# Optimization experiments

Hardware: AMD Instinct MI355X
Metric: run time of the kernel (lower is better)

## Reference

```python
import jax, jax.numpy as jnp
import numpy as np

BS, L, D, H, DC = 8, 8192, 128, 128, 128
C_CONST = 8.0  # rg-lru temperature constant


def _ln(x):
    # LayerNorm without scale/bias (use_bias=False, use_scale=False)
    m = jnp.mean(x, axis=-1, keepdims=True)
    v = jnp.mean(jnp.square(x - m), axis=-1, keepdims=True)
    return (x - m) * jax.lax.rsqrt(v + 1e-6)


def _affine(c, w, b):
    # Dense(features=1)(c)[:, :, None] -> (bs, 1, 1) broadcast scalar per sequence
    return (c @ w + b)[:, :, None]


def _combine(e1, e2):
    a1, b1 = e1
    a2, b2 = e2
    return (a1 * a2, a2 * b1 + b2)


def _linear_scan(a, b, reverse):
    # h_t = a_t * h_{t-1} + b_t (or h_{t+1} when reverse) along seq axis 1
    _, h = jax.lax.associative_scan(_combine, (a, b), axis=1, reverse=reverse)
    return h


def _forward(x, c, cln1_sw, cln1_sb, cln1_bw, cln1_bb, gate1_w, gate1_b,
             rnn_in_w, rnn_in_b, pos_emb, rnn_wi, rnn_bi, rnn_wr, rnn_br, rnn_a,
             rnn_out_w, rnn_out_b, cln2_sw, cln2_sb, cln2_bw, cln2_bb,
             gate2_w, gate2_b, mlp_w1, mlp_b1, mlp_w2, mlp_b2):
    # --- branch 1: conditioned LN -> bidirectional RG-LRU -> gated residual ---
    h = (1.0 + _affine(c, cln1_sw, cln1_sb)) * _ln(x) + _affine(c, cln1_bw, cln1_bb)
    u = _ln(h) @ rnn_in_w + rnn_in_b + pos_emb[None]          # (bs, L, H)
    gi = jax.nn.sigmoid(u @ rnn_wi + rnn_bi)                   # input gate
    gr = jax.nn.sigmoid(u @ rnn_wr + rnn_br)                   # recurrence gate
    at = jnp.exp(C_CONST * gr * jnp.log(rnn_a))                # a_t = a^(c*r_t)
    bt = jnp.sqrt(1.0 - jnp.square(at)) * (gi * u)
    hf = _linear_scan(at, bt, reverse=False)
    hb = _linear_scan(at, bt, reverse=True)
    r = jnp.concatenate([hf, hb], axis=-1) @ rnn_out_w + rnn_out_b  # (bs, L, D)
    x = x + _affine(c, gate1_w, gate1_b) * r
    # --- branch 2: conditioned LN -> gelu MLP -> gated residual ---
    h = (1.0 + _affine(c, cln2_sw, cln2_sb)) * _ln(x) + _affine(c, cln2_bw, cln2_bb)
    m = jax.nn.gelu(h @ mlp_w1 + mlp_b1) @ mlp_w2 + mlp_b2
    return x + _affine(c, gate2_w, gate2_b) * m


def setup_inputs() -> dict:
    key = jax.random.key(0)
    ks = jax.random.split(key, 30)
    def n(k, shape, s=0.05):
        return (jax.random.normal(k, shape) * s).astype(jnp.float32)
    rnn_a = (0.9 + 0.09 * jax.random.uniform(ks[0], (H,))).astype(jnp.float32)
    return {
        "x": jax.random.normal(ks[1], (BS, L, D), jnp.float32),
        "c": jax.random.normal(ks[2], (BS, DC), jnp.float32),
        "cln1_sw": n(ks[3], (DC, 1)), "cln1_sb": n(ks[4], (1,)),
        "cln1_bw": n(ks[5], (DC, 1)), "cln1_bb": n(ks[6], (1,)),
        "gate1_w": n(ks[7], (DC, 1)), "gate1_b": n(ks[8], (1,)),
        "rnn_in_w": n(ks[9], (D, H), 0.1), "rnn_in_b": n(ks[10], (H,)),
        "pos_emb": n(ks[11], (L, H), 0.02),
        "rnn_wi": n(ks[12], (H, H), 0.1), "rnn_bi": n(ks[13], (H,)),
        "rnn_wr": n(ks[14], (H, H), 0.1), "rnn_br": n(ks[15], (H,)),
        "rnn_a": rnn_a,
        "rnn_out_w": n(ks[16], (2 * H, D), 0.1), "rnn_out_b": n(ks[17], (D,)),
        "cln2_sw": n(ks[18], (DC, 1)), "cln2_sb": n(ks[19], (1,)),
        "cln2_bw": n(ks[20], (DC, 1)), "cln2_bb": n(ks[21], (1,)),
        "gate2_w": n(ks[22], (DC, 1)), "gate2_b": n(ks[23], (1,)),
        "mlp_w1": n(ks[24], (D, 4 * D), 0.1), "mlp_b1": n(ks[25], (4 * D,)),
        "mlp_w2": n(ks[26], (4 * D, D), 0.1), "mlp_b2": n(ks[27], (D,)),
    }


def reference(x, c, cln1_sw, cln1_sb, cln1_bw, cln1_bb, gate1_w, gate1_b,
              rnn_in_w, rnn_in_b, pos_emb, rnn_wi, rnn_bi, rnn_wr, rnn_br, rnn_a,
              rnn_out_w, rnn_out_b, cln2_sw, cln2_sb, cln2_bw, cln2_bb,
              gate2_w, gate2_b, mlp_w1, mlp_b1, mlp_w2, mlp_b2):
    return _forward(x, c, cln1_sw, cln1_sb, cln1_bw, cln1_bb, gate1_w, gate1_b,
                    rnn_in_w, rnn_in_b, pos_emb, rnn_wi, rnn_bi, rnn_wr, rnn_br, rnn_a,
                    rnn_out_w, rnn_out_b, cln2_sw, cln2_sb, cln2_bw, cln2_bb,
                    gate2_w, gate2_b, mlp_w1, mlp_b1, mlp_w2, mlp_b2)
```

## Files before the change

### kernel.cpp

```cpp
#include <hip/hip_runtime.h>
#include <hip/hip_bf16.h>

#define BSZ 8
#define SEQ 8192
#define DIM 128
#define NCH 128
#define CLEN 64

typedef unsigned short u16;
typedef unsigned int u32;
typedef short bf16x8 __attribute__((ext_vector_type(8)));
typedef float f32x4  __attribute__((ext_vector_type(4)));
typedef float f32x16 __attribute__((ext_vector_type(16)));

__device__ __forceinline__ float us2f(u16 w){ union{u32 i;float f;}u; u.i=((u32)w)<<16; return u.f; }
__device__ __forceinline__ u16 f2us(float f){
  __hip_bfloat16 h = __float2bfloat16(f);
  union{ __hip_bfloat16 b; u16 s; }u; u.b=h; return u.s;
}
__device__ __forceinline__ float wred64(float v){
  #pragma unroll
  for (int o=1;o<64;o<<=1) v += __shfl_xor(v,o,64);
  return v;
}
__device__ __forceinline__ float red16(float v){
  v += __shfl_xor(v,1,64); v += __shfl_xor(v,2,64);
  v += __shfl_xor(v,4,64); v += __shfl_xor(v,8,64);
  return v;
}
__device__ __forceinline__ float sigmoidf_(float z){ return 1.f/(1.f+__expf(-z)); }
__device__ __forceinline__ float gelu_tanh(float x){
  float y = 0.7978845608028654f * fmaf(0.044715f*x, x*x, x);
  float e = __expf(2.f*y);
  float th = 1.f - 2.f/(e+1.f);
  return 0.5f*x*(1.f+th);
}
__device__ __forceinline__ void lds_fence(){
  asm volatile("s_waitcnt lgkmcnt(0)" ::: "memory");
  __builtin_amdgcn_sched_barrier(0);
}

__global__ __launch_bounds__(64) void k_aff(
    const float* __restrict__ c,
    const float* w0,const float* w1,const float* w2,const float* w3,const float* w4,const float* w5,
    const float* s0,const float* s1,const float* s2,const float* s3,const float* s4,const float* s5,
    float* __restrict__ aff)
{
  const float* ws[6]={w0,w1,w2,w3,w4,w5};
  const float* bs[6]={s0,s1,s2,s3,s4,s5};
  int l = threadIdx.x;
  for (int b=0;b<BSZ;++b){
    #pragma unroll
    for (int h=0;h<6;++h){
      float v = c[b*128+l]*ws[h][l] + c[b*128+64+l]*ws[h][64+l];
      v = wred64(v);
      if (l==0) aff[b*6+h] = v + bs[h][0];
    }
  }
}

__device__ __forceinline__ void pack_one(const float* __restrict__ W, int N,
                                         u16* __restrict__ out, int fi)
{
  int lane = fi & 63;
  int k2   = (fi >> 6) & 1;
  int cn   = fi >> 7;
  int NB   = N >> 4;
  int n    = cn % NB, c = cn / NB;
  int k0   = c*64 + k2*32 + (lane>>4)*8;
  int col  = n*16 + (lane&15);
  u16* o = out + (size_t)fi*8;
  #pragma unroll
  for (int j=0;j<8;++j) o[j] = f2us(W[(size_t)(k0+j)*N + col]);
}

__device__ __forceinline__ void pack32A(const float* __restrict__ W, int N,
                                        u16* __restrict__ out, int fi)
{
  int lane = fi & 63;
  int ks   = (fi >> 6) & 7;
  int ng   = fi >> 9;
  int k0   = ks*16 + (lane>>5)*8;
  int col  = ng*32 + (lane&31);
  u16* o = out + (size_t)fi*8;
  #pragma unroll
  for (int j=0;j<8;++j) o[j] = f2us(W[(size_t)(k0+j)*N + col]);
}

__device__ __forceinline__ void pack32B(const float* __restrict__ W, int N,
                                        u16* __restrict__ out, int fi)
{
  int lane = fi & 63;
  int ot   = (fi >> 6) & 3;
  int ksg  = fi >> 8;
  int k0   = ksg*16 + (lane>>5)*8;
  int col  = ot*32 + (lane&31);
  u16* o = out + (size_t)fi*8;
  #pragma unroll
  for (int j=0;j<8;++j) o[j] = f2us(W[(size_t)(k0+j)*N + col]);
}

__global__ __launch_bounds__(256) void k_prep(
    const float* __restrict__ w1, const float* __restrict__ w2, const float* __restrict__ wo,
    const float* __restrict__ win, const float* __restrict__ wi, const float* __restrict__ wr,
    u16* __restrict__ w1t, u16* __restrict__ w2t, u16* __restrict__ wot,
    u16* __restrict__ wint, u16* __restrict__ wit, u16* __restrict__ wrt)
{
  int i = blockIdx.x*256 + threadIdx.x;
  if      (i <  8192) pack32A(w1, 512, w1t, i);
  else if (i < 16384) pack32B(w2, 128, w2t, i-8192);
  else if (i < 20480) pack_one(wo, 128, wot, i-16384);
  else if (i < 22528) pack_one(win,128, wint,i-20480);
  else if (i < 24576) pack_one(wi, 128, wit, i-22528);
  else                pack_one(wr, 128, wrt, i-24576);
}

__global__ __launch_bounds__(256,4) void k_pre(
    const float* __restrict__ xg, const u16* __restrict__ wint, const float* __restrict__ b_in,
    const float* __restrict__ pos, const u16* __restrict__ wit, const float* __restrict__ b_i,
    const u16* __restrict__ wrt, const float* __restrict__ b_r, const float* __restrict__ avec,
    const float* __restrict__ aff,
    u32* __restrict__ abg,
    float* __restrict__ Ag, float* __restrict__ Bfg, float* __restrict__ Bbg)
{
  __shared__ __align__(16) u32 abp[CLEN*DIM];
  u16* A_l = (u16*)abp;
  const int t  = threadIdx.x;
  const int b  = blockIdx.x >> 7;
  const int ck = blockIdx.x & (NCH-1);
  const size_t base = ((size_t)(b*SEQ + ck*CLEN))*DIM;
  const int lane=t&63, wv=t>>6, col=lane&15, quad=lane>>4;
  const int m0 = wv*16;

  {
    const float s1p = 1.f + aff[b*6+0];
    const int cg=t&15, rg=t>>4, j0=cg*8, r0=rg*4;
    #pragma unroll
    for (int ii=0;ii<4;++ii){
      int r=r0+ii;
      const float* xo = xg + base + (size_t)r*DIM + j0;
      float4 a = *(const float4*)xo;
      float4 bq = *(const float4*)(xo+4);
      float o[8]={a.x,a.y,a.z,a.w,bq.x,bq.y,bq.z,bq.w};
      float s=0.f;
      #pragma unroll
      for (int j=0;j<8;++j) s+=o[j];
      s=red16(s); float m=s*(1.f/128.f);
      float q2=0.f;
      #pragma unroll
      for (int j=0;j<8;++j){ float d=o[j]-m; q2+=d*d; }
      q2=red16(q2); float var=q2*(1.f/128.f);
      float rs=rsqrtf(var+1e-6f);
      float vz=var*rs*rs;
      float tt2=s1p*rsqrtf(fmaf(s1p*s1p,vz,1e-6f));
      float sc=rs*tt2;
      u32 pk[4];
      #pragma unroll
      for (int q=0;q<4;++q){
        pk[q]= (u32)f2us((o[2*q]-m)*sc) | ((u32)f2us((o[2*q+1]-m)*sc)<<16);
      }
      *(uint4*)&A_l[r*136+j0] = make_uint4(pk[0],pk[1],pk[2],pk[3]);
    }
  }
  lds_fence();

  f32x4 uacc[8];
  #pragma unroll
  for (int n=0;n<8;++n) uacc[n]=(f32x4){0.f,0.f,0.f,0.f};
  #pragma unroll
  for (int c=0;c<2;++c){
    #pragma unroll
    for (int k2=0;k2<2;++k2){
      bf16x8 av = *(const bf16x8*)&A_l[(m0+col)*136 + c*64 + k2*32 + quad*8];
      #pragma unroll
      for (int n=0;n<8;++n){
        bf16x8 bv = *(const bf16x8*)&wint[(size_t)(((c*8+n)*2+k2)*64+lane)*8];
        uacc[n] = __builtin_amdgcn_mfma_f32_16x16x32_bf16(av, bv, uacc[n], 0,0,0);
      }
    }
  }
  float u_c[8][4];
  #pragma unroll
  for (int n=0;n<8;++n){
    int nc = n*16 + col;
    float bi = b_in[nc];
    #pragma unroll
    for (int r=0;r<4;++r){
      int row = m0 + quad*4 + r;
      u_c[n][r] = uacc[n][r] + bi + pos[(size_t)(ck*CLEN+row)*DIM + nc];
    }
  }
  #pragma unroll
  for (int n=0;n<8;++n){
    #pragma unroll
    for (int r=0;r<4;++r)
      A_l[(m0+quad*4+r)*136 + n*16+col] = f2us(u_c[n][r]);
  }
  lds_fence();

  f32x4 gacc[8], racc[8];
  #pragma unroll
  for (int n=0;n<8;++n){ gacc[n]=(f32x4){0.f,0.f,0.f,0.f}; racc[n]=(f32x4){0.f,0.f,0.f,0.f}; }
  #pragma unroll
  for (int c=0;c<2;++c){
    #pragma unroll
    for (int k2=0;k2<2;++k2){
      bf16x8 av = *(const bf16x8*)&A_l[(m0+col)*136 + c*64 + k2*32 + quad*8];
      #pragma unroll
      for (int n=0;n<8;++n){
        bf16x8 bgi = *(const bf16x8*)&wit[(size_t)(((c*8+n)*2+k2)*64+lane)*8];
        gacc[n] = __builtin_amdgcn_mfma_f32_16x16x32_bf16(av, bgi, gacc[n], 0,0,0);
        bf16x8 bgr = *(const bf16x8*)&wrt[(size_t)(((c*8+n)*2+k2)*64+lane)*8];
        racc[n] = __builtin_amdgcn_mfma_f32_16x16x32_bf16(av, bgr, racc[n], 0,0,0);
      }
    }
  }
  __syncthreads();

  #pragma unroll
  for (int n=0;n<8;++n){
    int nc = n*16 + col;
    float la = __logf(avec[nc]);
    float br = b_r[nc];
    float bi = b_i[nc];
    #pragma unroll
    for (int r=0;r<4;++r){
      int row = m0 + quad*4 + r;
      float gi = sigmoidf_(gacc[n][r]+bi);
      float g  = sigmoidf_(racc[n][r]+br);
      float a  = __expf(8.f*g*la);
      float bb = sqrtf(fmaxf(1.f-a*a,0.f))*gi*u_c[n][r];
      abp[row*DIM+nc] = (u32)f2us(a) | ((u32)f2us(bb)<<16);
    }
  }
  __syncthreads();

  {
    uint4* dst = (uint4*)(abg + base);
    const uint4* src = (const uint4*)abp;
    #pragma unroll
    for (int i=t;i<2048;i+=256) dst[i]=src[i];
  }

  const int sbase = (b*NCH+ck)*DIM;
  if (t < 128){
    float h=0.f, p=1.f;
    #pragma unroll 4
    for (int tt=0;tt<CLEN;++tt){
      u32 v=abp[tt*DIM+t];
      float a=us2f((u16)v), bb=us2f((u16)(v>>16));
      h=fmaf(a,h,bb); p*=a;
    }
    Ag[sbase+t]=p; Bfg[sbase+t]=h;
  } else {
    int ch=t-128; float h=0.f;
    #pragma unroll 4
    for (int tt=CLEN-1;tt>=0;--tt){
      u32 v=abp[tt*DIM+ch];
      h=fmaf(us2f((u16)v),h,us2f((u16)(v>>16)));
    }
    Bbg[sbase+ch]=h;
  }
}

__global__ __launch_bounds__(1024) void k_chunkscan(
    const float* __restrict__ Ag, const float* __restrict__ Bfg, const float* __restrict__ Bbg,
    float* __restrict__ Hf, float* __restrict__ Hb)
{
  __shared__ float sP[8][128], sS[8][128];
  const int dir = blockIdx.x >> 3, b = blockIdx.x & 7;
  const int t = threadIdx.x, seg = t>>7, ch = t&127;
  const size_t cbase = (size_t)b*NCH*DIM + ch;
  float P=1.f, S=0.f;
  if (dir==0){
    #pragma unroll 4
    for (int j=0;j<16;++j){
      size_t i = cbase + (size_t)(seg*16+j)*DIM;
      float a=Ag[i]; S=fmaf(a,S,Bfg[i]); P*=a;
    }
  } else {
    #pragma unroll 4
    for (int j=15;j>=0;--j){
      size_t i = cbase + (size_t)(seg*16+j)*DIM;
      float a=Ag[i]; S=fmaf(a,S,Bbg[i]); P*=a;
    }
  }
  sP[seg][ch]=P; sS[seg][ch]=S;
  __syncthreads();
  float h=0.f;
  if (dir==0){ for (int s=0;s<seg;++s) h=fmaf(sP[s][ch],h,sS[s][ch]); }
  else       { for (int s=7;s>seg;--s) h=fmaf(sP[s][ch],h,sS[s][ch]); }
  if (dir==0){
    #pragma unroll 4
    for (int j=0;j<16;++j){
      size_t i = cbase + (size_t)(seg*16+j)*DIM;
      Hf[i]=h; h=fmaf(Ag[i],h,Bfg[i]);
    }
  } else {
    #pragma unroll 4
    for (int j=15;j>=0;--j){
      size_t i = cbase + (size_t)(seg*16+j)*DIM;
      Hb[i]=h; h=fmaf(Ag[i],h,Bbg[i]);
    }
  }
}

__global__ __launch_bounds__(256,4) void k_scan(
    const u32* __restrict__ abg,
    const float* __restrict__ Hf, const float* __restrict__ Hb,
    const float* __restrict__ xg, const u16* __restrict__ wot, const float* __restrict__ b_out,
    const float* __restrict__ aff, float* __restrict__ outg)
{
  __shared__ __align__(16) u16 hcat[CLEN*264];
  const int t  = threadIdx.x;
  const int b  = blockIdx.x >> 7;
  const int ck = blockIdx.x & (NCH-1);
  const size_t base = ((size_t)(b*SEQ + ck*CLEN))*DIM;
  const int pbase=(b*NCH+ck)*DIM;

  if (t<128){
    const u32* p = abg + base + t;
    float h = Hf[pbase+t];
    u32 v0=p[0], v1=p[128], v2=p[256], v3=p[384];
    #pragma unroll
    for (int g=0; g<16; ++g){
      u32 n0=0,n1=0,n2=0,n3=0;
      if (g<15){
        n0=p[(g*4+4)*128]; n1=p[(g*4+5)*128];
        n2=p[(g*4+6)*128]; n3=p[(g*4+7)*128];
      }
      h=fmaf(us2f((u16)v0),h,us2f((u16)(v0>>16))); hcat[(g*4+0)*264+t]=f2us(h);
      h=fmaf(us2f((u16)v1),h,us2f((u16)(v1>>16))); hcat[(g*4+1)*264+t]=f2us(h);
      h=fmaf(us2f((u16)v2),h,us2f((u16)(v2>>16))); hcat[(g*4+2)*264+t]=f2us(h);
      h=fmaf(us2f((u16)v3),h,us2f((u16)(v3>>16))); hcat[(g*4+3)*264+t]=f2us(h);
      v0=n0; v1=n1; v2=n2; v3=n3;
    }
  } else {
    int ch=t-128;
    const u32* p = abg + base + ch;
    float h = Hb[pbase+ch];
    u32 v0=p[63*128], v1=p[62*128], v2=p[61*128], v3=p[60*128];
    #pragma unroll
    for (int g=0; g<16; ++g){
      u32 n0=0,n1=0,n2=0,n3=0;
      if (g<15){
        n0=p[(59-g*4)*128]; n1=p[(58-g*4)*128];
        n2=p[(57-g*4)*128]; n3=p[(56-g*4)*128];
      }
      h=fmaf(us2f((u16)v0),h,us2f((u16)(v0>>16))); hcat[(63-g*4)*264+128+ch]=f2us(h);
      h=fmaf(us2f((u16)v1),h,us2f((u16)(v1>>16))); hcat[(62-g*4)*264+128+ch]=f2us(h);
      h=fmaf(us2f((u16)v2),h,us2f((u16)(v2>>16))); hcat[(61-g*4)*264+128+ch]=f2us(h);
      h=fmaf(us2f((u16)v3),h,us2f((u16)(v3>>16))); hcat[(60-g*4)*264+128+ch]=f2us(h);
      v0=n0; v1=n1; v2=n2; v3=n3;
    }
  }
  __syncthreads();

  const int lane=t&63, wv=t>>6, col=lane&15, quad=lane>>4;
  const int m0 = wv*16;
  f32x4 acc[8];
  #pragma unroll
  for (int n=0;n<8;++n) acc[n]=(f32x4){0.f,0.f,0.f,0.f};
  #pragma unroll
  for (int chk=0; chk<4; ++chk){
    #pragma unroll
    for (int k2=0;k2<2;++k2){
      bf16x8 av = *(const bf16x8*)&hcat[(m0+col)*264 + chk*64 + k2*32 + quad*8];
      #pragma unroll
      for (int n=0;n<8;++n){
        bf16x8 bv = *(const bf16x8*)&wot[(size_t)(((chk*8+n)*2+k2)*64+lane)*8];
        acc[n] = __builtin_amdgcn_mfma_f32_16x16x32_bf16(av, bv, acc[n], 0,0,0);
      }
    }
  }
  __syncthreads();
  float* pbuf = (float*)hcat;
  #pragma unroll
  for (int n=0;n<8;++n){
    #pragma unroll
    for (int r=0;r<4;++r)
      pbuf[(m0+quad*4+r)*128 + n*16+col] = acc[n][r];
  }
  __syncthreads();

  const float g1=aff[b*6+2];
  const float4* xv4 = (const float4*)(xg+base);
  float4* ov4 = (float4*)(outg+base);
  const float4* cv4 = (const float4*)pbuf;
  #pragma unroll
  for (int i=t;i<2048;i+=256){
    float4 cv = cv4[i];
    float4 xv = xv4[i];
    float4 bo = *(const float4*)&b_out[(i*4)&127];
    float4 r;
    r.x=fmaf(g1,cv.x+bo.x,xv.x); r.y=fmaf(g1,cv.y+bo.y,xv.y);
    r.z=fmaf(g1,cv.z+bo.z,xv.z); r.w=fmaf(g1,cv.w+bo.w,xv.w);
    ov4[i]=r;
  }
}

__global__ __launch_bounds__(256,2) void k_mlp(
    const u16* __restrict__ w1t, const float* __restrict__ b1v,
    const u16* __restrict__ w2t, const float* __restrict__ b2v,
    const float* __restrict__ aff, float* __restrict__ outg)
{
  __shared__ __align__(16) u32 smem4[8192];
  u16* h2l = (u16*)smem4;
  const int t=threadIdx.x;
  const int b=blockIdx.x>>7;
  const size_t base=(size_t)blockIdx.x*CLEN*DIM;
  const int lane=t&63, wv=t>>6;
  const int l31=lane&31, h5=lane>>5;
  const float s2p=1.f+aff[b*6+3], b2a=aff[b*6+4], g2=aff[b*6+5];

  {
    const int cg=t&15, rg=t>>4, j0=cg*8, r0=rg*4;
    #pragma unroll
    for (int ii=0;ii<4;++ii){
      int r=r0+ii;
      const float* xo = outg + base + (size_t)r*DIM + j0;
      float4 a = *(const float4*)xo;
      float4 bq = *(const float4*)(xo+4);
      float o[8]={a.x,a.y,a.z,a.w,bq.x,bq.y,bq.z,bq.w};
      float s=0.f;
      #pragma unroll
      for (int j=0;j<8;++j) s+=o[j];
      s=red16(s); float m=s*(1.f/128.f);
      float q2=0.f;
      #pragma unroll
      for (int j=0;j<8;++j){ float d=o[j]-m; q2+=d*d; }
      q2=red16(q2); float rs=rsqrtf(q2*(1.f/128.f)+1e-6f);
      u32 pk[4];
      #pragma unroll
      for (int q=0;q<4;++q){
        float a0=fmaf((o[2*q]-m)*rs,   s2p, b2a);
        float a1=fmaf((o[2*q+1]-m)*rs, s2p, b2a);
        pk[q]= (u32)f2us(a0) | ((u32)f2us(a1)<<16);
      }
      *(uint4*)&h2l[r*136+j0] = make_uint4(pk[0],pk[1],pk[2],pk[3]);
    }
  }
  __syncthreads();

  f32x16 acc2[2][4];
  #pragma unroll
  for (int m=0;m<2;++m)
    #pragma unroll
    for (int n=0;n<4;++n)
      #pragma unroll
      for (int r=0;r<16;++r) acc2[m][n][r]=0.f;

  for (int nt=0;nt<4;++nt){
    bf16x8 w1A[8];
    #pragma unroll
    for (int ks=0;ks<8;++ks)
      w1A[ks] = *(const bf16x8*)&w1t[((size_t)((wv*4+nt)*8 + ks)*64 + lane)*8];
    #pragma unroll
    for (int tt=0;tt<2;++tt){
      f32x16 a1;
      #pragma unroll
      for (int r=0;r<16;++r) a1[r]=0.f;
      #pragma unroll
      for (int ks=0;ks<8;++ks){
        bf16x8 hb = *(const bf16x8*)&h2l[(tt*32 + l31)*136 + ks*16 + h5*8];
        a1 = __builtin_amdgcn_mfma_f32_32x32x16_bf16(w1A[ks], hb, a1, 0,0,0);
      }
      u32 pk[8];
      #pragma unroll
      for (int q=0;q<4;++q){
        float4 bq = *(const float4*)&b1v[wv*128 + nt*32 + q*8 + h5*4];
        float g0=gelu_tanh(a1[4*q+0]+bq.x);
        float g1=gelu_tanh(a1[4*q+1]+bq.y);
        float g2_=gelu_tanh(a1[4*q+2]+bq.z);
        float g3=gelu_tanh(a1[4*q+3]+bq.w);
        pk[2*q+0]=(u32)f2us(g0)|((u32)f2us(g1)<<16);
        pk[2*q+1]=(u32)f2us(g2_)|((u32)f2us(g3)<<16);
      }
      asm volatile("v_permlane32_swap_b32 %0, %1" : "+v"(pk[0]), "+v"(pk[2]));
      asm volatile("v_permlane32_swap_b32 %0, %1" : "+v"(pk[1]), "+v"(pk[3]));
      asm volatile("v_permlane32_swap_b32 %0, %1" : "+v"(pk[4]), "+v"(pk[6]));
      asm volatile("v_permlane32_swap_b32 %0, %1" : "+v"(pk[5]), "+v"(pk[7]));
      union F8 { bf16x8 v; u32 u[4]; } A0, A1;
      A0.u[0]=pk[0]; A0.u[1]=pk[1]; A0.u[2]=pk[2]; A0.u[3]=pk[3];
      A1.u[0]=pk[4]; A1.u[1]=pk[5]; A1.u[2]=pk[6]; A1.u[3]=pk[7];
      #pragma unroll
      for (int ot=0;ot<4;++ot){
        bf16x8 wb0 = *(const bf16x8*)&w2t[((size_t)((wv*8 + nt*2 + 0)*4 + ot)*64 + lane)*8];
        acc2[tt][ot] = __builtin_amdgcn_mfma_f32_32x32x16_bf16(A0.v, wb0, acc2[tt][ot], 0,0,0);
        bf16x8 wb1 = *(const bf16x8*)&w2t[((size_t)((wv*8 + nt*2 + 1)*4 + ot)*64 + lane)*8];
        acc2[tt][ot] = __builtin_amdgcn_mfma_f32_32x32x16_bf16(A1.v, wb1, acc2[tt][ot], 0,0,0);
      }
    }
  }
  __syncthreads();

  float* pbuf = (float*)smem4;
  const int lrow = (lane>>4)&3;
  const int cb   = (lane&15)*8;
  #pragma unroll
  for (int rt=0;rt<4;++rt){
    const int tt = rt>>1, gg = rt&1;
    if (rt) __syncthreads();
    #pragma unroll
    for (int ot=0;ot<4;++ot){
      #pragma unroll
      for (int q=0;q<2;++q){
        #pragma unroll
        for (int r=0;r<4;++r){
          int reg = gg*8 + q*4 + r;
          int tl  = q*8 + r + 4*h5;
          pbuf[wv*2048 + tl*128 + ot*32 + l31] = acc2[tt][ot][reg];
        }
      }
    }
    __syncthreads();
    float s[8] = {0.f,0.f,0.f,0.f,0.f,0.f,0.f,0.f};
    #pragma unroll
    for (int p=0;p<4;++p){
      float4 x0 = *(const float4*)&pbuf[p*2048 + (4*wv+lrow)*128 + cb];
      float4 x1 = *(const float4*)&pbuf[p*2048 + (4*wv+lrow)*128 + cb + 4];
      s[0]+=x0.x; s[1]+=x0.y; s[2]+=x0.z; s[3]+=x0.w;
      s[4]+=x1.x; s[5]+=x1.y; s[6]+=x1.z; s[7]+=x1.w;
    }
    int grow = rt*16 + 4*wv + lrow;
    size_t gi = base + (size_t)grow*DIM + cb;
    float4 o0 = *(const float4*)&outg[gi];
    float4 o1 = *(const float4*)&outg[gi+4];
    float4 bb0 = *(const float4*)&b2v[cb];
    float4 bb1 = *(const float4*)&b2v[cb+4];
    float4 r0, r1;
    r0.x = fmaf(g2, s[0]+bb0.x, o0.x); r0.y = fmaf(g2, s[1]+bb0.y, o0.y);
    r0.z = fmaf(g2, s[2]+bb0.z, o0.z); r0.w = fmaf(g2, s[3]+bb0.w, o0.w);
    r1.x = fmaf(g2, s[4]+bb1.x, o1.x); r1.y = fmaf(g2, s[5]+bb1.y, o1.y);
    r1.z = fmaf(g2, s[6]+bb1.z, o1.z); r1.w = fmaf(g2, s[7]+bb1.w, o1.w);
    *(float4*)&outg[gi]   = r0;
    *(float4*)&outg[gi+4] = r1;
  }
}

extern "C" void kernel_launch(void* const* d_in, const int* in_sizes, int n_in,
                              void* d_out, int out_size, void* d_ws, size_t ws_size,
                              hipStream_t stream)
{
  (void)in_sizes; (void)n_in; (void)out_size; (void)ws_size;
  const float* x   =(const float*)d_in[0];
  const float* c   =(const float*)d_in[1];
  const float* c1sw=(const float*)d_in[2];  const float* c1sb=(const float*)d_in[3];
  const float* c1bw=(const float*)d_in[4];  const float* c1bb=(const float*)d_in[5];
  const float* g1w =(const float*)d_in[6];  const float* g1b =(const float*)d_in[7];
  const float* win =(const float*)d_in[8];  const float* binv=(const float*)d_in[9];
  const float* pos =(const float*)d_in[10];
  const float* wi  =(const float*)d_in[11]; const float* biv =(const float*)d_in[12];
  const float* wr  =(const float*)d_in[13]; const float* brv =(const float*)d_in[14];
  const float* av  =(const float*)d_in[15];
  const float* wout=(const float*)d_in[16]; const float* bout=(const float*)d_in[17];
  const float* c2sw=(const float*)d_in[18]; const float* c2sb=(const float*)d_in[19];
  const float* c2bw=(const float*)d_in[20]; const float* c2bb=(const float*)d_in[21];
  const float* g2w =(const float*)d_in[22]; const float* g2b =(const float*)d_in[23];
  const float* w1  =(const float*)d_in[24]; const float* b1v =(const float*)d_in[25];
  const float* w2  =(const float*)d_in[26]; const float* b2v =(const float*)d_in[27];

  float* wsf  = (float*)d_ws;
  float* Ag   = wsf;
  float* Bfg  = Ag   + 131072;
  float* Bbg  = Bfg  + 131072;
  float* Hf   = Bbg  + 131072;
  float* Hb   = Hf   + 131072;
  float* aff  = Hb   + 131072;
  u16*   w1t  = (u16*)(aff + 64);
  u16*   w2t  = w1t + 65536;
  u16*   wot  = w2t + 65536;
  u16*   wint = wot + 32768;
  u16*   wit  = wint + 16384;
  u16*   wrt  = wit  + 16384;
  u32*   abg  = (u32*)(wrt + 16384);

  float* outg = (float*)d_out;

  k_aff<<<dim3(1),dim3(64),0,stream>>>(c, c1sw,c1bw,g1w,c2sw,c2bw,g2w,
                                       c1sb,c1bb,g1b,c2sb,c2bb,g2b, aff);
  k_prep<<<dim3(104),dim3(256),0,stream>>>(w1,w2,wout,win,wi,wr,
                                           w1t,w2t,wot,wint,wit,wrt);
  k_pre<<<dim3(BSZ*NCH),dim3(256),0,stream>>>(x,wint,binv,pos,wit,biv,wrt,brv,av,aff,
                                              abg, Ag,Bfg,Bbg);
  k_chunkscan<<<dim3(16),dim3(1024),0,stream>>>(Ag,Bfg,Bbg,Hf,Hb);
  k_scan<<<dim3(BSZ*NCH),dim3(256),0,stream>>>(abg,Hf,Hb,x,wot,bout,aff,outg);
  k_mlp<<<dim3(BSZ*NCH),dim3(256),0,stream>>>(w1t,b1v,w2t,b2v,aff,outg);
}
```

Measured before the change: 272.6 us.

## Restructure MLP kernel so each wave owns 32 rows with full hidden dim

The MLP kernel now gives each wave 32 rows and loops over all 512 hidden units, instead of splitting the hidden dimension across waves. This removes the cross-wave LDS reduction and its block barriers, and the residual is written straight from the accumulators. Each block covers 128 rows, so half as many blocks are launched. The affine kernel is also folded into the weight-prep launch as an extra block, saving one launch. The cost is that each wave now reads the whole W1/W2 from global/L2, which is more weight traffic per row, and the output stores are scattered at float granularity.

```diff
diff --git a/kernel.cpp b/kernel.cpp
--- a/kernel.cpp
+++ b/kernel.cpp
@@ -38,25 +38,6 @@
 __device__ __forceinline__ void lds_fence(){
   asm volatile("s_waitcnt lgkmcnt(0)" ::: "memory");
   __builtin_amdgcn_sched_barrier(0);
-}
-
-__global__ __launch_bounds__(64) void k_aff(
-    const float* __restrict__ c,
-    const float* w0,const float* w1,const float* w2,const float* w3,const float* w4,const float* w5,
-    const float* s0,const float* s1,const float* s2,const float* s3,const float* s4,const float* s5,
-    float* __restrict__ aff)
-{
-  const float* ws[6]={w0,w1,w2,w3,w4,w5};
-  const float* bs[6]={s0,s1,s2,s3,s4,s5};
-  int l = threadIdx.x;
-  for (int b=0;b<BSZ;++b){
-    #pragma unroll
-    for (int h=0;h<6;++h){
-      float v = c[b*128+l]*ws[h][l] + c[b*128+64+l]*ws[h][64+l];
-      v = wred64(v);
-      if (l==0) aff[b*6+h] = v + bs[h][0];
-    }
-  }
 }
 
 __device__ __forceinline__ void pack_one(const float* __restrict__ W, int N,
@@ -104,8 +85,28 @@
     const float* __restrict__ w1, const float* __restrict__ w2, const float* __restrict__ wo,
     const float* __restrict__ win, const float* __restrict__ wi, const float* __restrict__ wr,
     u16* __restrict__ w1t, u16* __restrict__ w2t, u16* __restrict__ wot,
-    u16* __restrict__ wint, u16* __restrict__ wit, u16* __restrict__ wrt)
-{
+    u16* __restrict__ wint, u16* __restrict__ wit, u16* __restrict__ wrt,
+    const float* __restrict__ c,
+    const float* a0,const float* a1,const float* a2,const float* a3,const float* a4,const float* a5,
+    const float* s0,const float* s1,const float* s2,const float* s3,const float* s4,const float* s5,
+    float* __restrict__ aff)
+{
+  if (blockIdx.x == 104){
+    int l = threadIdx.x;
+    if (l < 64){
+      const float* ws[6]={a0,a1,a2,a3,a4,a5};
+      const float* bs[6]={s0,s1,s2,s3,s4,s5};
+      for (int b=0;b<BSZ;++b){
+        #pragma unroll
+        for (int h=0;h<6;++h){
+          float v = c[b*128+l]*ws[h][l] + c[b*128+64+l]*ws[h][64+l];
+          v = wred64(v);
+          if (l==0) aff[b*6+h] = v + bs[h][0];
+        }
+      }
+    }
+    return;
+  }
   int i = blockIdx.x*256 + threadIdx.x;
   if      (i <  8192) pack32A(w1, 512, w1t, i);
   else if (i < 16384) pack32B(w2, 128, w2t, i-8192);
@@ -404,21 +405,22 @@
     const u16* __restrict__ w2t, const float* __restrict__ b2v,
     const float* __restrict__ aff, float* __restrict__ outg)
 {
-  __shared__ __align__(16) u32 smem4[8192];
-  u16* h2l = (u16*)smem4;
+  __shared__ __align__(16) u16 h2l[4*32*136];
   const int t=threadIdx.x;
-  const int b=blockIdx.x>>7;
-  const size_t base=(size_t)blockIdx.x*CLEN*DIM;
+  const int b=blockIdx.x>>6;
+  const size_t base=(size_t)blockIdx.x*128*DIM;
   const int lane=t&63, wv=t>>6;
   const int l31=lane&31, h5=lane>>5;
   const float s2p=1.f+aff[b*6+3], b2a=aff[b*6+4], g2=aff[b*6+5];
+  u16* h2w = h2l + wv*32*136;
+  const size_t wbase = base + (size_t)wv*32*DIM;
 
   {
-    const int cg=t&15, rg=t>>4, j0=cg*8, r0=rg*4;
-    #pragma unroll
-    for (int ii=0;ii<4;++ii){
-      int r=r0+ii;
-      const float* xo = outg + base + (size_t)r*DIM + j0;
+    const int cg=lane&15, rg=lane>>4, j0=cg*8;
+    #pragma unroll
+    for (int ii=0;ii<8;++ii){
+      int r=rg*8+ii;
+      const float* xo = outg + wbase + (size_t)r*DIM + j0;
       float4 a = *(const float4*)xo;
       float4 bq = *(const float4*)(xo+4);
       float o[8]={a.x,a.y,a.z,a.w,bq.x,bq.y,bq.z,bq.w};
@@ -437,104 +439,68 @@
         float a1=fmaf((o[2*q+1]-m)*rs, s2p, b2a);
         pk[q]= (u32)f2us(a0) | ((u32)f2us(a1)<<16);
       }
-      *(uint4*)&h2l[r*136+j0] = make_uint4(pk[0],pk[1],pk[2],pk[3]);
-    }
-  }
-  __syncthreads();
-
-  f32x16 acc2[2][4];
-  #pragma unroll
-  for (int m=0;m<2;++m)
-    #pragma unroll
-    for (int n=0;n<4;++n)
-      #pragma unroll
-      for (int r=0;r<16;++r) acc2[m][n][r]=0.f;
-
-  for (int nt=0;nt<4;++nt){
+      *(uint4*)&h2w[r*136+j0] = make_uint4(pk[0],pk[1],pk[2],pk[3]);
+    }
+  }
+  lds_fence();
+
+  f32x16 acc2[4];
+  #pragma unroll
+  for (int n=0;n<4;++n)
+    #pragma unroll
+    for (int r=0;r<16;++r) acc2[n][r]=0.f;
+
+  for (int nt=0;nt<16;++nt){
     bf16x8 w1A[8];
     #pragma unroll
     for (int ks=0;ks<8;++ks)
-      w1A[ks] = *(const bf16x8*)&w1t[((size_t)((wv*4+nt)*8 + ks)*64 + lane)*8];
-    #pragma unroll
-    for (int tt=0;tt<2;++tt){
-      f32x16 a1;
-      #pragma unroll
-      for (int r=0;r<16;++r) a1[r]=0.f;
-      #pragma unroll
-      for (int ks=0;ks<8;++ks){
-        bf16x8 hb = *(const bf16x8*)&h2l[(tt*32 + l31)*136 + ks*16 + h5*8];
-        a1 = __builtin_amdgcn_mfma_f32_32x32x16_bf16(w1A[ks], hb, a1, 0,0,0);
-      }
-      u32 pk[8];
-      #pragma unroll
-      for (int q=0;q<4;++q){
-        float4 bq = *(const float4*)&b1v[wv*128 + nt*32 + q*8 + h5*4];
-        float g0=gelu_tanh(a1[4*q+0]+bq.x);
-        float g1=gelu_tanh(a1[4*q+1]+bq.y);
-        float g2_=gelu_tanh(a1[4*q+2]+bq.z);
-        float g3=gelu_tanh(a1[4*q+3]+bq.w);
-        pk[2*q+0]=(u32)f2us(g0)|((u32)f2us(g1)<<16);
-        pk[2*q+1]=(u32)f2us(g2_)|((u32)f2us(g3)<<16);
-      }
-      asm volatile("v_permlane32_swap_b32 %0, %1" : "+v"(pk[0]), "+v"(pk[2]));
-      asm volatile("v_permlane32_swap_b32 %0, %1" : "+v"(pk[1]), "+v"(pk[3]));
-      asm volatile("v_permlane32_swap_b32 %0, %1" : "+v"(pk[4]), "+v"(pk[6]));
-      asm volatile("v_permlane32_swap_b32 %0, %1" : "+v"(pk[5]), "+v"(pk[7]));
-      union F8 { bf16x8 v; u32 u[4]; } A0, A1;
-      A0.u[0]=pk[0]; A0.u[1]=pk[1]; A0.u[2]=pk[2]; A0.u[3]=pk[3];
-      A1.u[0]=pk[4]; A1.u[1]=pk[5]; A1.u[2]=pk[6]; A1.u[3]=pk[7];
-      #pragma unroll
-      for (int ot=0;ot<4;++ot){
-        bf16x8 wb0 = *(const bf16x8*)&w2t[((size_t)((wv*8 + nt*2 + 0)*4 + ot)*64 + lane)*8];
-        acc2[tt][ot] = __builtin_amdgcn_mfma_f32_32x32x16_bf16(A0.v, wb0, acc2[tt][ot], 0,0,0);
-        bf16x8 wb1 = *(const bf16x8*)&w2t[((size_t)((wv*8 + nt*2 + 1)*4 + ot)*64 + lane)*8];
-        acc2[tt][ot] = __builtin_amdgcn_mfma_f32_32x32x16_bf16(A1.v, wb1, acc2[tt][ot], 0,0,0);
-      }
-    }
-  }
-  __syncthreads();
-
-  float* pbuf = (float*)smem4;
-  const int lrow = (lane>>4)&3;
-  const int cb   = (lane&15)*8;
-  #pragma unroll
-  for (int rt=0;rt<4;++rt){
-    const int tt = rt>>1, gg = rt&1;
-    if (rt) __syncthreads();
+      w1A[ks] = *(const bf16x8*)&w1t[((size_t)(nt*8 + ks)*64 + lane)*8];
+    f32x16 a1a, a1b;
+    #pragma unroll
+    for (int r=0;r<16;++r){ a1a[r]=0.f; a1b[r]=0.f; }
+    #pragma unroll
+    for (int ks=0;ks<4;++ks){
+      bf16x8 hb0 = *(const bf16x8*)&h2w[l31*136 + (2*ks+0)*16 + h5*8];
+      a1a = __builtin_amdgcn_mfma_f32_32x32x16_bf16(w1A[2*ks+0], hb0, a1a, 0,0,0);
+      bf16x8 hb1 = *(const bf16x8*)&h2w[l31*136 + (2*ks+1)*16 + h5*8];
+      a1b = __builtin_amdgcn_mfma_f32_32x32x16_bf16(w1A[2*ks+1], hb1, a1b, 0,0,0);
+    }
+    u32 pk[8];
+    #pragma unroll
+    for (int q=0;q<4;++q){
+      float4 bq = *(const float4*)&b1v[nt*32 + q*8 + h5*4];
+      float g0=gelu_tanh(a1a[4*q+0]+a1b[4*q+0]+bq.x);
+      float g1=gelu_tanh(a1a[4*q+1]+a1b[4*q+1]+bq.y);
+      float g2_=gelu_tanh(a1a[4*q+2]+a1b[4*q+2]+bq.z);
+      float g3=gelu_tanh(a1a[4*q+3]+a1b[4*q+3]+bq.w);
+      pk[2*q+0]=(u32)f2us(g0)|((u32)f2us(g1)<<16);
+      pk[2*q+1]=(u32)f2us(g2_)|((u32)f2us(g3)<<16);
+    }
+    asm volatile("v_permlane32_swap_b32 %0, %1" : "+v"(pk[0]), "+v"(pk[2]));
+    asm volatile("v_permlane32_swap_b32 %0, %1" : "+v"(pk[1]), "+v"(pk[3]));
+    asm volatile("v_permlane32_swap_b32 %0, %1" : "+v"(pk[4]), "+v"(pk[6]));
+    asm volatile("v_permlane32_swap_b32 %0, %1" : "+v"(pk[5]), "+v"(pk[7]));
+    union F8 { bf16x8 v; u32 u[4]; } A0, A1;
+    A0.u[0]=pk[0]; A0.u[1]=pk[1]; A0.u[2]=pk[2]; A0.u[3]=pk[3];
+    A1.u[0]=pk[4]; A1.u[1]=pk[5]; A1.u[2]=pk[6]; A1.u[3]=pk[7];
     #pragma unroll
     for (int ot=0;ot<4;++ot){
-      #pragma unroll
-      for (int q=0;q<2;++q){
-        #pragma unroll
-        for (int r=0;r<4;++r){
-          int reg = gg*8 + q*4 + r;
-          int tl  = q*8 + r + 4*h5;
-          pbuf[wv*2048 + tl*128 + ot*32 + l31] = acc2[tt][ot][reg];
-        }
-      }
-    }
-    __syncthreads();
-    float s[8] = {0.f,0.f,0.f,0.f,0.f,0.f,0.f,0.f};
-    #pragma unroll
-    for (int p=0;p<4;++p){
-      float4 x0 = *(const float4*)&pbuf[p*2048 + (4*wv+lrow)*128 + cb];
-      float4 x1 = *(const float4*)&pbuf[p*2048 + (4*wv+lrow)*128 + cb + 4];
-      s[0]+=x0.x; s[1]+=x0.y; s[2]+=x0.z; s[3]+=x0.w;
-      s[4]+=x1.x; s[5]+=x1.y; s[6]+=x1.z; s[7]+=x1.w;
-    }
-    int grow = rt*16 + 4*wv + lrow;
-    size_t gi = base + (size_t)grow*DIM + cb;
-    float4 o0 = *(const float4*)&outg[gi];
-    float4 o1 = *(const float4*)&outg[gi+4];
-    float4 bb0 = *(const float4*)&b2v[cb];
-    float4 bb1 = *(const float4*)&b2v[cb+4];
-    float4 r0, r1;
-    r0.x = fmaf(g2, s[0]+bb0.x, o0.x); r0.y = fmaf(g2, s[1]+bb0.y, o0.y);
-    r0.z = fmaf(g2, s[2]+bb0.z, o0.z); r0.w = fmaf(g2, s[3]+bb0.w, o0.w);
-    r1.x = fmaf(g2, s[4]+bb1.x, o1.x); r1.y = fmaf(g2, s[5]+bb1.y, o1.y);
-    r1.z = fmaf(g2, s[6]+bb1.z, o1.z); r1.w = fmaf(g2, s[7]+bb1.w, o1.w);
-    *(float4*)&outg[gi]   = r0;
-    *(float4*)&outg[gi+4] = r1;
+      bf16x8 wb0 = *(const bf16x8*)&w2t[((size_t)((nt*2 + 0)*4 + ot)*64 + lane)*8];
+      acc2[ot] = __builtin_amdgcn_mfma_f32_32x32x16_bf16(A0.v, wb0, acc2[ot], 0,0,0);
+      bf16x8 wb1 = *(const bf16x8*)&w2t[((size_t)((nt*2 + 1)*4 + ot)*64 + lane)*8];
+      acc2[ot] = __builtin_amdgcn_mfma_f32_32x32x16_bf16(A1.v, wb1, acc2[ot], 0,0,0);
+    }
+  }
+
+  #pragma unroll
+  for (int ot=0;ot<4;++ot){
+    float bb = b2v[ot*32 + l31];
+    #pragma unroll
+    for (int reg=0;reg<16;++reg){
+      int row = (reg&3) + 8*(reg>>2) + 4*h5;
+      size_t gi = wbase + (size_t)row*DIM + ot*32 + l31;
+      outg[gi] = fmaf(g2, acc2[ot][reg] + bb, outg[gi]);
+    }
   }
 }
 
@@ -577,13 +543,13 @@
 
   float* outg = (float*)d_out;
 
-  k_aff<<<dim3(1),dim3(64),0,stream>>>(c, c1sw,c1bw,g1w,c2sw,c2bw,g2w,
-                                       c1sb,c1bb,g1b,c2sb,c2bb,g2b, aff);
-  k_prep<<<dim3(104),dim3(256),0,stream>>>(w1,w2,wout,win,wi,wr,
-                                           w1t,w2t,wot,wint,wit,wrt);
+  k_prep<<<dim3(105),dim3(256),0,stream>>>(w1,w2,wout,win,wi,wr,
+                                           w1t,w2t,wot,wint,wit,wrt,
+                                           c, c1sw,c1bw,g1w,c2sw,c2bw,g2w,
+                                           c1sb,c1bb,g1b,c2sb,c2bb,g2b, aff);
   k_pre<<<dim3(BSZ*NCH),dim3(256),0,stream>>>(x,wint,binv,pos,wit,biv,wrt,brv,av,aff,
                                               abg, Ag,Bfg,Bbg);
   k_chunkscan<<<dim3(16),dim3(1024),0,stream>>>(Ag,Bfg,Bbg,Hf,Hb);
   k_scan<<<dim3(BSZ*NCH),dim3(256),0,stream>>>(abg,Hf,Hb,x,wot,bout,aff,outg);
-  k_mlp<<<dim3(BSZ*NCH),dim3(256),0,stream>>>(w1t,b1v,w2t,b2v,aff,outg);
-}
+  k_mlp<<<dim3(BSZ*64),dim3(256),0,stream>>>(w1t,b1v,w2t,b2v,aff,outg);
+}
```

Result: slower. 291.2 us (+6.8%).

## Fuse RNN output projection with MLP kernel and fold affine into prep

Applied to the files above, without the earlier changes.

The scan/output-projection kernel and the MLP kernel become one kernel. The residual x is normalized straight from registers for the second branch instead of being re-read from global memory. The per-sequence affine computation moves into an extra block of the weight-prep launch, removing a tiny separate kernel launch. The first MLP GEMM now loads weights inline and splits the K loop over two accumulators for more MFMA independence. The fused kernel is capped at two blocks per CU, so the scan phase runs at lower occupancy than before.

```diff
diff --git a/kernel.cpp b/kernel.cpp
--- a/kernel.cpp
+++ b/kernel.cpp
@@ -38,25 +38,6 @@
 __device__ __forceinline__ void lds_fence(){
   asm volatile("s_waitcnt lgkmcnt(0)" ::: "memory");
   __builtin_amdgcn_sched_barrier(0);
-}
-
-__global__ __launch_bounds__(64) void k_aff(
-    const float* __restrict__ c,
-    const float* w0,const float* w1,const float* w2,const float* w3,const float* w4,const float* w5,
-    const float* s0,const float* s1,const float* s2,const float* s3,const float* s4,const float* s5,
-    float* __restrict__ aff)
-{
-  const float* ws[6]={w0,w1,w2,w3,w4,w5};
-  const float* bs[6]={s0,s1,s2,s3,s4,s5};
-  int l = threadIdx.x;
-  for (int b=0;b<BSZ;++b){
-    #pragma unroll
-    for (int h=0;h<6;++h){
-      float v = c[b*128+l]*ws[h][l] + c[b*128+64+l]*ws[h][64+l];
-      v = wred64(v);
-      if (l==0) aff[b*6+h] = v + bs[h][0];
-    }
-  }
 }
 
 __device__ __forceinline__ void pack_one(const float* __restrict__ W, int N,
@@ -104,8 +85,28 @@
     const float* __restrict__ w1, const float* __restrict__ w2, const float* __restrict__ wo,
     const float* __restrict__ win, const float* __restrict__ wi, const float* __restrict__ wr,
     u16* __restrict__ w1t, u16* __restrict__ w2t, u16* __restrict__ wot,
-    u16* __restrict__ wint, u16* __restrict__ wit, u16* __restrict__ wrt)
-{
+    u16* __restrict__ wint, u16* __restrict__ wit, u16* __restrict__ wrt,
+    const float* __restrict__ c,
+    const float* a0,const float* a1,const float* a2,const float* a3,const float* a4,const float* a5,
+    const float* s0,const float* s1,const float* s2,const float* s3,const float* s4,const float* s5,
+    float* __restrict__ aff)
+{
+  if (blockIdx.x == 104){
+    int l = threadIdx.x;
+    if (l < 64){
+      const float* ws[6]={a0,a1,a2,a3,a4,a5};
+      const float* bs[6]={s0,s1,s2,s3,s4,s5};
+      for (int b=0;b<BSZ;++b){
+        #pragma unroll
+        for (int h=0;h<6;++h){
+          float v = c[b*128+l]*ws[h][l] + c[b*128+64+l]*ws[h][64+l];
+          v = wred64(v);
+          if (l==0) aff[b*6+h] = v + bs[h][0];
+        }
+      }
+    }
+    return;
+  }
   int i = blockIdx.x*256 + threadIdx.x;
   if      (i <  8192) pack32A(w1, 512, w1t, i);
   else if (i < 16384) pack32B(w2, 128, w2t, i-8192);
@@ -305,13 +306,18 @@
   }
 }
 
-__global__ __launch_bounds__(256,4) void k_scan(
+__global__ __launch_bounds__(256,2) void k_fuse(
     const u32* __restrict__ abg,
     const float* __restrict__ Hf, const float* __restrict__ Hb,
     const float* __restrict__ xg, const u16* __restrict__ wot, const float* __restrict__ b_out,
+    const u16* __restrict__ w1t, const float* __restrict__ b1v,
+    const u16* __restrict__ w2t, const float* __restrict__ b2v,
     const float* __restrict__ aff, float* __restrict__ outg)
 {
-  __shared__ __align__(16) u16 hcat[CLEN*264];
+  __shared__ __align__(16) u16 smem[CLEN*264];
+  u16* hcat = smem;
+  float* pbuf = (float*)smem;
+  u16* h2l = smem;
   const int t  = threadIdx.x;
   const int b  = blockIdx.x >> 7;
   const int ck = blockIdx.x & (NCH-1);
@@ -358,90 +364,76 @@
 
   const int lane=t&63, wv=t>>6, col=lane&15, quad=lane>>4;
   const int m0 = wv*16;
-  f32x4 acc[8];
-  #pragma unroll
-  for (int n=0;n<8;++n) acc[n]=(f32x4){0.f,0.f,0.f,0.f};
-  #pragma unroll
-  for (int chk=0; chk<4; ++chk){
-    #pragma unroll
-    for (int k2=0;k2<2;++k2){
-      bf16x8 av = *(const bf16x8*)&hcat[(m0+col)*264 + chk*64 + k2*32 + quad*8];
-      #pragma unroll
-      for (int n=0;n<8;++n){
-        bf16x8 bv = *(const bf16x8*)&wot[(size_t)(((chk*8+n)*2+k2)*64+lane)*8];
-        acc[n] = __builtin_amdgcn_mfma_f32_16x16x32_bf16(av, bv, acc[n], 0,0,0);
-      }
-    }
-  }
-  __syncthreads();
-  float* pbuf = (float*)hcat;
-  #pragma unroll
-  for (int n=0;n<8;++n){
-    #pragma unroll
-    for (int r=0;r<4;++r)
-      pbuf[(m0+quad*4+r)*128 + n*16+col] = acc[n][r];
+  {
+    f32x4 acc[8];
+    #pragma unroll
+    for (int n=0;n<8;++n) acc[n]=(f32x4){0.f,0.f,0.f,0.f};
+    #pragma unroll
+    for (int chk=0; chk<4; ++chk){
+      #pragma unroll
+      for (int k2=0;k2<2;++k2){
+        bf16x8 av = *(const bf16x8*)&hcat[(m0+col)*264 + chk*64 + k2*32 + quad*8];
+        #pragma unroll
+        for (int n=0;n<8;++n){
+          bf16x8 bv = *(const bf16x8*)&wot[(size_t)(((chk*8+n)*2+k2)*64+lane)*8];
+          acc[n] = __builtin_amdgcn_mfma_f32_16x16x32_bf16(av, bv, acc[n], 0,0,0);
+        }
+      }
+    }
+    __syncthreads();
+    #pragma unroll
+    for (int n=0;n<8;++n){
+      #pragma unroll
+      for (int r=0;r<4;++r)
+        pbuf[(m0+quad*4+r)*128 + n*16+col] = acc[n][r];
+    }
   }
   __syncthreads();
 
   const float g1=aff[b*6+2];
-  const float4* xv4 = (const float4*)(xg+base);
-  float4* ov4 = (float4*)(outg+base);
-  const float4* cv4 = (const float4*)pbuf;
-  #pragma unroll
-  for (int i=t;i<2048;i+=256){
-    float4 cv = cv4[i];
-    float4 xv = xv4[i];
-    float4 bo = *(const float4*)&b_out[(i*4)&127];
-    float4 r;
-    r.x=fmaf(g1,cv.x+bo.x,xv.x); r.y=fmaf(g1,cv.y+bo.y,xv.y);
-    r.z=fmaf(g1,cv.z+bo.z,xv.z); r.w=fmaf(g1,cv.w+bo.w,xv.w);
-    ov4[i]=r;
-  }
-}
-
-__global__ __launch_bounds__(256,2) void k_mlp(
-    const u16* __restrict__ w1t, const float* __restrict__ b1v,
-    const u16* __restrict__ w2t, const float* __restrict__ b2v,
-    const float* __restrict__ aff, float* __restrict__ outg)
-{
-  __shared__ __align__(16) u32 smem4[8192];
-  u16* h2l = (u16*)smem4;
-  const int t=threadIdx.x;
-  const int b=blockIdx.x>>7;
-  const size_t base=(size_t)blockIdx.x*CLEN*DIM;
-  const int lane=t&63, wv=t>>6;
+  const float s2p=1.f+aff[b*6+3], b2a=aff[b*6+4], g2=aff[b*6+5];
+  const int cg=t&15, rg=t>>4, j0=cg*8, r0=rg*4;
+  u32 pkh[4][4];
+  #pragma unroll
+  for (int ii=0;ii<4;++ii){
+    int r=r0+ii;
+    const float* xi = xg + base + (size_t)r*DIM + j0;
+    float4 xa = *(const float4*)xi;
+    float4 xb = *(const float4*)(xi+4);
+    float4 ca = *(const float4*)&pbuf[r*128+j0];
+    float4 cb = *(const float4*)&pbuf[r*128+j0+4];
+    float4 ba = *(const float4*)&b_out[j0];
+    float4 bbv = *(const float4*)&b_out[j0+4];
+    float o[8];
+    o[0]=fmaf(g1,ca.x+ba.x,xa.x); o[1]=fmaf(g1,ca.y+ba.y,xa.y);
+    o[2]=fmaf(g1,ca.z+ba.z,xa.z); o[3]=fmaf(g1,ca.w+ba.w,xa.w);
+    o[4]=fmaf(g1,cb.x+bbv.x,xb.x); o[5]=fmaf(g1,cb.y+bbv.y,xb.y);
+    o[6]=fmaf(g1,cb.z+bbv.z,xb.z); o[7]=fmaf(g1,cb.w+bbv.w,xb.w);
+    float* xo = outg + base + (size_t)r*DIM + j0;
+    *(float4*)xo     = make_float4(o[0],o[1],o[2],o[3]);
+    *(float4*)(xo+4) = make_float4(o[4],o[5],o[6],o[7]);
+    float s=0.f;
+    #pragma unroll
+    for (int j=0;j<8;++j) s+=o[j];
+    s=red16(s); float m=s*(1.f/128.f);
+    float q2=0.f;
+    #pragma unroll
+    for (int j=0;j<8;++j){ float d=o[j]-m; q2+=d*d; }
+    q2=red16(q2); float rs=rsqrtf(q2*(1.f/128.f)+1e-6f);
+    #pragma unroll
+    for (int q=0;q<4;++q){
+      float a0=fmaf((o[2*q]-m)*rs,   s2p, b2a);
+      float a1=fmaf((o[2*q+1]-m)*rs, s2p, b2a);
+      pkh[ii][q]= (u32)f2us(a0) | ((u32)f2us(a1)<<16);
+    }
+  }
+  __syncthreads();
+  #pragma unroll
+  for (int ii=0;ii<4;++ii)
+    *(uint4*)&h2l[(r0+ii)*136+j0] = make_uint4(pkh[ii][0],pkh[ii][1],pkh[ii][2],pkh[ii][3]);
+  __syncthreads();
+
   const int l31=lane&31, h5=lane>>5;
-  const float s2p=1.f+aff[b*6+3], b2a=aff[b*6+4], g2=aff[b*6+5];
-
-  {
-    const int cg=t&15, rg=t>>4, j0=cg*8, r0=rg*4;
-    #pragma unroll
-    for (int ii=0;ii<4;++ii){
-      int r=r0+ii;
-      const float* xo = outg + base + (size_t)r*DIM + j0;
-      float4 a = *(const float4*)xo;
-      float4 bq = *(const float4*)(xo+4);
-      float o[8]={a.x,a.y,a.z,a.w,bq.x,bq.y,bq.z,bq.w};
-      float s=0.f;
-      #pragma unroll
-      for (int j=0;j<8;++j) s+=o[j];
-      s=red16(s); float m=s*(1.f/128.f);
-      float q2=0.f;
-      #pragma unroll
-      for (int j=0;j<8;++j){ float d=o[j]-m; q2+=d*d; }
-      q2=red16(q2); float rs=rsqrtf(q2*(1.f/128.f)+1e-6f);
-      u32 pk[4];
-      #pragma unroll
-      for (int q=0;q<4;++q){
-        float a0=fmaf((o[2*q]-m)*rs,   s2p, b2a);
-        float a1=fmaf((o[2*q+1]-m)*rs, s2p, b2a);
-        pk[q]= (u32)f2us(a0) | ((u32)f2us(a1)<<16);
-      }
-      *(uint4*)&h2l[r*136+j0] = make_uint4(pk[0],pk[1],pk[2],pk[3]);
-    }
-  }
-  __syncthreads();
-
   f32x16 acc2[2][4];
   #pragma unroll
   for (int m=0;m<2;++m)
@@ -450,30 +442,41 @@
       #pragma unroll
       for (int r=0;r<16;++r) acc2[m][n][r]=0.f;
 
-  for (int nt=0;nt<4;++nt){
-    bf16x8 w1A[8];
-    #pragma unroll
-    for (int ks=0;ks<8;++ks)
-      w1A[ks] = *(const bf16x8*)&w1t[((size_t)((wv*4+nt)*8 + ks)*64 + lane)*8];
+  for (int s=0;s<4;++s){
+    f32x4 dummy_;
+    (void)dummy_;
+    bf16x8 w1A0[8];
+    #pragma unroll
+    for (int ks=0;ks<8;++ks){
+      int kk = ks>>1, k2 = ks&1;
+      (void)kk; (void)k2;
+    }
     #pragma unroll
     for (int tt=0;tt<2;++tt){
       f32x16 a1;
       #pragma unroll
       for (int r=0;r<16;++r) a1[r]=0.f;
-      #pragma unroll
-      for (int ks=0;ks<8;++ks){
-        bf16x8 hb = *(const bf16x8*)&h2l[(tt*32 + l31)*136 + ks*16 + h5*8];
-        a1 = __builtin_amdgcn_mfma_f32_32x32x16_bf16(w1A[ks], hb, a1, 0,0,0);
+      f32x16 a1b;
+      #pragma unroll
+      for (int r=0;r<16;++r) a1b[r]=0.f;
+      #pragma unroll
+      for (int ks=0;ks<4;++ks){
+        bf16x8 wa0 = *(const bf16x8*)&w1t[((size_t)((wv*4 + s)*8 + 2*ks+0)*64 + lane)*8];
+        bf16x8 hb0 = *(const bf16x8*)&h2l[(tt*32 + l31)*136 + (2*ks+0)*16 + h5*8];
+        a1 = __builtin_amdgcn_mfma_f32_32x32x16_bf16(wa0, hb0, a1, 0,0,0);
+        bf16x8 wa1 = *(const bf16x8*)&w1t[((size_t)((wv*4 + s)*8 + 2*ks+1)*64 + lane)*8];
+        bf16x8 hb1 = *(const bf16x8*)&h2l[(tt*32 + l31)*136 + (2*ks+1)*16 + h5*8];
+        a1b = __builtin_amdgcn_mfma_f32_32x32x16_bf16(wa1, hb1, a1b, 0,0,0);
       }
       u32 pk[8];
       #pragma unroll
       for (int q=0;q<4;++q){
-        float4 bq = *(const float4*)&b1v[wv*128 + nt*32 + q*8 + h5*4];
-        float g0=gelu_tanh(a1[4*q+0]+bq.x);
-        float g1=gelu_tanh(a1[4*q+1]+bq.y);
-        float g2_=gelu_tanh(a1[4*q+2]+bq.z);
-        float g3=gelu_tanh(a1[4*q+3]+bq.w);
-        pk[2*q+0]=(u32)f2us(g0)|((u32)f2us(g1)<<16);
+        float4 bq = *(const float4*)&b1v[(wv*4+s)*32 + q*8 + h5*4];
+        float g0=gelu_tanh(a1[4*q+0]+a1b[4*q+0]+bq.x);
+        float g1_=gelu_tanh(a1[4*q+1]+a1b[4*q+1]+bq.y);
+        float g2_=gelu_tanh(a1[4*q+2]+a1b[4*q+2]+bq.z);
+        float g3=gelu_tanh(a1[4*q+3]+a1b[4*q+3]+bq.w);
+        pk[2*q+0]=(u32)f2us(g0)|((u32)f2us(g1_)<<16);
         pk[2*q+1]=(u32)f2us(g2_)|((u32)f2us(g3)<<16);
       }
       asm volatile("v_permlane32_swap_b32 %0, %1" : "+v"(pk[0]), "+v"(pk[2]));
@@ -485,16 +488,15 @@
       A1.u[0]=pk[4]; A1.u[1]=pk[5]; A1.u[2]=pk[6]; A1.u[3]=pk[7];
       #pragma unroll
       for (int ot=0;ot<4;++ot){
-        bf16x8 wb0 = *(const bf16x8*)&w2t[((size_t)((wv*8 + nt*2 + 0)*4 + ot)*64 + lane)*8];
+        bf16x8 wb0 = *(const bf16x8*)&w2t[((size_t)(((wv*4+s)*2 + 0)*4 + ot)*64 + lane)*8];
         acc2[tt][ot] = __builtin_amdgcn_mfma_f32_32x32x16_bf16(A0.v, wb0, acc2[tt][ot], 0,0,0);
-        bf16x8 wb1 = *(const bf16x8*)&w2t[((size_t)((wv*8 + nt*2 + 1)*4 + ot)*64 + lane)*8];
+        bf16x8 wb1 = *(const bf16x8*)&w2t[((size_t)(((wv*4+s)*2 + 1)*4 + ot)*64 + lane)*8];
         acc2[tt][ot] = __builtin_amdgcn_mfma_f32_32x32x16_bf16(A1.v, wb1, acc2[tt][ot], 0,0,0);
       }
     }
   }
   __syncthreads();
 
-  float* pbuf = (float*)smem4;
   const int lrow = (lane>>4)&3;
   const int cb   = (lane&15)*8;
   #pragma unroll
@@ -577,13 +579,13 @@
 
   float* outg = (float*)d_out;
 
-  k_aff<<<dim3(1),dim3(64),0,stream>>>(c, c1sw,c1bw,g1w,c2sw,c2bw,g2w,
-                                       c1sb,c1bb,g1b,c2sb,c2bb,g2b, aff);
-  k_prep<<<dim3(104),dim3(256),0,stream>>>(w1,w2,wout,win,wi,wr,
-                                           w1t,w2t,wot,wint,wit,wrt);
+  k_prep<<<dim3(105),dim3(256),0,stream>>>(w1,w2,wout,win,wi,wr,
+                                           w1t,w2t,wot,wint,wit,wrt,
+                                           c, c1sw,c1bw,g1w,c2sw,c2bw,g2w,
+                                           c1sb,c1bb,g1b,c2sb,c2bb,g2b, aff);
   k_pre<<<dim3(BSZ*NCH),dim3(256),0,stream>>>(x,wint,binv,pos,wit,biv,wrt,brv,av,aff,
                                               abg, Ag,Bfg,Bbg);
   k_chunkscan<<<dim3(16),dim3(1024),0,stream>>>(Ag,Bfg,Bbg,Hf,Hb);
-  k_scan<<<dim3(BSZ*NCH),dim3(256),0,stream>>>(abg,Hf,Hb,x,wot,bout,aff,outg);
-  k_mlp<<<dim3(BSZ*NCH),dim3(256),0,stream>>>(w1t,b1v,w2t,b2v,aff,outg);
-}
+  k_fuse<<<dim3(BSZ*NCH),dim3(256),0,stream>>>(abg,Hf,Hb,x,wot,bout,
+                                               w1t,b1v,w2t,b2v,aff,outg);
+}
```

After: 276.4 us. About the same (+1.4%).
